# Kernel tuning notes

Hardware: AMD Instinct MI355X
Metric: run time of the kernel (lower is better)

The kernel has to match this reference:

```python
import math
import jax, jax.numpy as jnp
from jax import lax
import numpy as np

B, S, H, D = 2, 2048, 8, 32
Q_CHUNK = 64  # query-block size; keeps the [b,chunk,t,h,d] diff tensor ~256 MB


def setup_inputs() -> dict:
    key = jax.random.key(0)
    kq, kk = jax.random.split(key)
    q = jax.random.normal(kq, (B, S, H, D), dtype=jnp.float32)
    k = jax.random.normal(kk, (B, S, H, D), dtype=jnp.float32)
    return {"q": q, "k": k}


def _l1_scores(q, k):
    # q, k: [b, s, h, d] -> attn: [b, s, t, h]
    b, s, h, d = q.shape
    scale = 1.0 / math.sqrt(d)
    n_chunks = s // Q_CHUNK
    # [n_chunks, b, Q_CHUNK, h, d]
    q_blocks = jnp.moveaxis(q.reshape(b, n_chunks, Q_CHUNK, h, d), 1, 0)

    def step(carry, q_blk):
        # q_blk: [b, c, h, d]; k: [b, t, h, d]
        # diff: [b, c, t, h, d] -> reduce over d
        dist = jnp.sum(jnp.abs(q_blk[:, :, None, :, :] - k[:, None, :, :, :]), axis=-1)
        return carry, -dist * scale  # [b, c, t, h]

    _, out = lax.scan(step, None, q_blocks)  # [n_chunks, b, c, t, h]
    return jnp.moveaxis(out, 0, 1).reshape(b, s, s, h)


def reference(q, k):
    return _l1_scores(q, k)
```

## Files before the change

kernel.cpp:

```cpp
#include <hip/hip_runtime.h>
#include <cstdint>
#include <cstddef>


#define S_DIM 2048
#define H_DIM 8
#define D_DIM 32
#define RS 4
#define SB 16
#define TSPLIT 4
#define TCHUNK 8
#define NTHREADS 256
#define NCH ((S_DIM / TSPLIT) / TCHUNK)

typedef float f32x4 __attribute__((ext_vector_type(4)));

__global__ __launch_bounds__(NTHREADS) void l1attn_kernel(
    const float* __restrict__ q, const float* __restrict__ k,
    float* __restrict__ out)
{
  __shared__ float ldsk[TCHUNK * H_DIM * D_DIM];

  const int tid  = threadIdx.x;
  const int lane = tid & 63;
  const int wave = tid >> 6;

  const int bid = blockIdx.x;
  const int b   = bid >> 9;
  const int rem = bid & 511;
  const int sg  = rem >> 2;
  const int tq  = rem & 3;

  const int h      = lane & 7;
  const int t_sub  = lane >> 3;
  const int s_base = sg * SB + wave * RS;
  const int t0     = tq * (S_DIM / TSPLIT);

  f32x4 qf[RS][8];
  {
    const float* qb = q + (size_t)b * S_DIM * (H_DIM * D_DIM);
#pragma unroll
    for (int i = 0; i < RS; ++i) {
      const float* qr = qb + (size_t)(s_base + i) * (H_DIM * D_DIM) + h * D_DIM;
#pragma unroll
      for (int dv = 0; dv < 8; ++dv)
        qf[i][dv] = *(const f32x4*)(qr + dv * 4);
    }
  }

  const float* kb = k + (size_t)b * S_DIM * (H_DIM * D_DIM);

  const int g4a = tid;
  const int g4b = tid + 256;
  const int f4a = (g4a & 7) * 64 + (g4a >> 3);
  const int f4b = (g4b & 7) * 64 + (g4b >> 3);

  const f32x4* kc0 = (const f32x4*)(kb + (size_t)t0 * (H_DIM * D_DIM));
  f32x4 st0 = kc0[g4a];
  f32x4 st1 = kc0[g4b];

  const float nscale = -0.17677669529663687f;
  float* optr = out +
      ((size_t)(b * S_DIM + s_base) * S_DIM + (size_t)(t0 + t_sub)) * H_DIM + h;

  f32x4* ldsv = (f32x4*)ldsk;

  for (int c = 0; c < NCH; ++c) {
    __syncthreads();

    ldsv[f4a] = st0;
    ldsv[f4b] = st1;

    if (c + 1 < NCH) {
      const f32x4* kn = (const f32x4*)(kb +
          (size_t)(t0 + (c + 1) * TCHUNK) * (H_DIM * D_DIM));
      st0 = kn[g4a];
      st1 = kn[g4b];
    }

    __syncthreads();

    float acc0 = 0.f, acc1 = 0.f, acc2 = 0.f, acc3 = 0.f;
#pragma unroll
    for (int dv = 0; dv < 8; ++dv) {
      const f32x4 kf = ldsv[dv * 64 + lane];
      acc0 += __builtin_fabsf(qf[0][dv].x - kf.x) + __builtin_fabsf(qf[0][dv].y - kf.y)
            + __builtin_fabsf(qf[0][dv].z - kf.z) + __builtin_fabsf(qf[0][dv].w - kf.w);
      acc1 += __builtin_fabsf(qf[1][dv].x - kf.x) + __builtin_fabsf(qf[1][dv].y - kf.y)
            + __builtin_fabsf(qf[1][dv].z - kf.z) + __builtin_fabsf(qf[1][dv].w - kf.w);
      acc2 += __builtin_fabsf(qf[2][dv].x - kf.x) + __builtin_fabsf(qf[2][dv].y - kf.y)
            + __builtin_fabsf(qf[2][dv].z - kf.z) + __builtin_fabsf(qf[2][dv].w - kf.w);
      acc3 += __builtin_fabsf(qf[3][dv].x - kf.x) + __builtin_fabsf(qf[3][dv].y - kf.y)
            + __builtin_fabsf(qf[3][dv].z - kf.z) + __builtin_fabsf(qf[3][dv].w - kf.w);
    }

    float* o = optr + (size_t)c * (TCHUNK * H_DIM);
    o[0]                         = acc0 * nscale;
    o[(size_t)1 * S_DIM * H_DIM] = acc1 * nscale;
    o[(size_t)2 * S_DIM * H_DIM] = acc2 * nscale;
    o[(size_t)3 * S_DIM * H_DIM] = acc3 * nscale;
  }
}

extern "C" void kernel_launch(void* const* d_in, const int* in_sizes, int n_in,
                              void* d_out, int out_size, void* d_ws, size_t ws_size,
                              hipStream_t stream) {
  const float* q = (const float*)d_in[0];
  const float* k = (const float*)d_in[1];
  float* out = (float*)d_out;
  const int B = 2;
  dim3 grid(B * (S_DIM / SB) * TSPLIT);
  dim3 block(NTHREADS);
  l1attn_kernel<<<grid, block, 0, stream>>>(q, k, out);
}
```

Baseline: 375.2 us.

## Double-buffer K tiles in LDS, swizzle layout, and split keys eight ways

Replaces the single LDS K tile with two ping-pong buffers. Each iteration stages the next chunk while the current one is consumed, so one of the two barriers per iteration goes away. The LDS layout changes from a transposed store to a rotated (swizzled) row layout, which aims to cut bank conflicts on the staging writes. The key dimension is split eight ways instead of four, doubling the grid for more parallelism, at the cost of twice the LDS space per block and more Q reloads.

```diff
diff --git a/kernel.cpp b/kernel.cpp
--- a/kernel.cpp
+++ b/kernel.cpp
@@ -8,7 +8,7 @@
 #define D_DIM 32
 #define RS 4
 #define SB 16
-#define TSPLIT 4
+#define TSPLIT 8
 #define TCHUNK 8
 #define NTHREADS 256
 #define NCH ((S_DIM / TSPLIT) / TCHUNK)
@@ -19,17 +19,17 @@
     const float* __restrict__ q, const float* __restrict__ k,
     float* __restrict__ out)
 {
-  __shared__ float ldsk[TCHUNK * H_DIM * D_DIM];
+  __shared__ float ldsk[2][TCHUNK * H_DIM * D_DIM];
 
   const int tid  = threadIdx.x;
   const int lane = tid & 63;
   const int wave = tid >> 6;
 
   const int bid = blockIdx.x;
-  const int b   = bid >> 9;
-  const int rem = bid & 511;
-  const int sg  = rem >> 2;
-  const int tq  = rem & 3;
+  const int b   = bid >> 10;
+  const int rem = bid & 1023;
+  const int sg  = rem >> 3;
+  const int tq  = rem & 7;
 
   const int h      = lane & 7;
   const int t_sub  = lane >> 3;
@@ -52,38 +52,52 @@
 
   const int g4a = tid;
   const int g4b = tid + 256;
-  const int f4a = (g4a & 7) * 64 + (g4a >> 3);
-  const int f4b = (g4b & 7) * 64 + (g4b >> 3);
+  const int f4a = ((g4a >> 3) << 3) | (((g4a & 7) + (g4a >> 3)) & 7);
+  const int f4b = ((g4b >> 3) << 3) | (((g4b & 7) + (g4b >> 3)) & 7);
 
-  const f32x4* kc0 = (const f32x4*)(kb + (size_t)t0 * (H_DIM * D_DIM));
-  f32x4 st0 = kc0[g4a];
-  f32x4 st1 = kc0[g4b];
+  int raddr[8];
+#pragma unroll
+  for (int dv = 0; dv < 8; ++dv)
+    raddr[dv] = (lane << 3) | ((dv + lane) & 7);
+
+  f32x4 st0, st1;
+  {
+    const f32x4* kc0 = (const f32x4*)(kb + (size_t)t0 * (H_DIM * D_DIM));
+    st0 = kc0[g4a];
+    st1 = kc0[g4b];
+    f32x4* b0 = (f32x4*)ldsk[0];
+    b0[f4a] = st0;
+    b0[f4b] = st1;
+    const f32x4* kc1 = (const f32x4*)(kb +
+        (size_t)(t0 + TCHUNK) * (H_DIM * D_DIM));
+    st0 = kc1[g4a];
+    st1 = kc1[g4b];
+  }
 
   const float nscale = -0.17677669529663687f;
   float* optr = out +
       ((size_t)(b * S_DIM + s_base) * S_DIM + (size_t)(t0 + t_sub)) * H_DIM + h;
 
-  f32x4* ldsv = (f32x4*)ldsk;
-
   for (int c = 0; c < NCH; ++c) {
     __syncthreads();
 
-    ldsv[f4a] = st0;
-    ldsv[f4b] = st1;
-
     if (c + 1 < NCH) {
-      const f32x4* kn = (const f32x4*)(kb +
-          (size_t)(t0 + (c + 1) * TCHUNK) * (H_DIM * D_DIM));
-      st0 = kn[g4a];
-      st1 = kn[g4b];
+      f32x4* nb = (f32x4*)ldsk[(c + 1) & 1];
+      nb[f4a] = st0;
+      nb[f4b] = st1;
+      if (c + 2 < NCH) {
+        const f32x4* kn = (const f32x4*)(kb +
+            (size_t)(t0 + (c + 2) * TCHUNK) * (H_DIM * D_DIM));
+        st0 = kn[g4a];
+        st1 = kn[g4b];
+      }
     }
 
-    __syncthreads();
-
+    const f32x4* kp = (const f32x4*)ldsk[c & 1];
     float acc0 = 0.f, acc1 = 0.f, acc2 = 0.f, acc3 = 0.f;
 #pragma unroll
     for (int dv = 0; dv < 8; ++dv) {
-      const f32x4 kf = ldsv[dv * 64 + lane];
+      const f32x4 kf = kp[raddr[dv]];
       acc0 += __builtin_fabsf(qf[0][dv].x - kf.x) + __builtin_fabsf(qf[0][dv].y - kf.y)
             + __builtin_fabsf(qf[0][dv].z - kf.z) + __builtin_fabsf(qf[0][dv].w - kf.w);
       acc1 += __builtin_fabsf(qf[1][dv].x - kf.x) + __builtin_fabsf(qf[1][dv].y - kf.y)
```

After: 351.3 us. 6.4% less time.

## Use single-wave workgroups with private K staging and swizzled LDS layout

Applied to the files above, without the earlier changes.

Each 256-thread block with four waves sharing one K chunk becomes a single 64-lane wave. That wave loads the whole K chunk itself into a swizzled LDS layout meant to avoid bank conflicts. The two __syncthreads per chunk become wave barriers, and the grid is split eight ways along t instead of four. This removes cross-wave barrier stalls, but each wave now fetches its own K data, so K traffic to L2 rises about fourfold.

```diff
diff --git a/kernel.cpp b/kernel.cpp
--- a/kernel.cpp
+++ b/kernel.cpp
@@ -7,10 +7,9 @@
 #define H_DIM 8
 #define D_DIM 32
 #define RS 4
-#define SB 16
-#define TSPLIT 4
+#define TSPLIT 8
 #define TCHUNK 8
-#define NTHREADS 256
+#define NTHREADS 64
 #define NCH ((S_DIM / TSPLIT) / TCHUNK)
 
 typedef float f32x4 __attribute__((ext_vector_type(4)));
@@ -19,21 +18,18 @@
     const float* __restrict__ q, const float* __restrict__ k,
     float* __restrict__ out)
 {
-  __shared__ float ldsk[TCHUNK * H_DIM * D_DIM];
+  __shared__ f32x4 ldsk[TCHUNK * H_DIM * D_DIM / 4];
 
-  const int tid  = threadIdx.x;
-  const int lane = tid & 63;
-  const int wave = tid >> 6;
+  const int lane = threadIdx.x;
 
   const int bid = blockIdx.x;
-  const int b   = bid >> 9;
-  const int rem = bid & 511;
-  const int sg  = rem >> 2;
-  const int tq  = rem & 3;
+  const int b   = bid >> 12;
+  const int tq  = (bid >> 9) & 7;
+  const int sg  = bid & 511;
 
   const int h      = lane & 7;
   const int t_sub  = lane >> 3;
-  const int s_base = sg * SB + wave * RS;
+  const int s_base = sg * RS;
   const int t0     = tq * (S_DIM / TSPLIT);
 
   f32x4 qf[RS][8];
@@ -41,49 +37,53 @@
     const float* qb = q + (size_t)b * S_DIM * (H_DIM * D_DIM);
 #pragma unroll
     for (int i = 0; i < RS; ++i) {
-      const float* qr = qb + (size_t)(s_base + i) * (H_DIM * D_DIM) + h * D_DIM;
+      const f32x4* qr = (const f32x4*)(qb +
+          (size_t)(s_base + i) * (H_DIM * D_DIM) + h * D_DIM);
 #pragma unroll
       for (int dv = 0; dv < 8; ++dv)
-        qf[i][dv] = *(const f32x4*)(qr + dv * 4);
+        qf[i][dv] = qr[dv];
     }
   }
 
-  const float* kb = k + (size_t)b * S_DIM * (H_DIM * D_DIM);
+  const f32x4* kbv = (const f32x4*)(k + (size_t)b * S_DIM * (H_DIM * D_DIM));
 
-  const int g4a = tid;
-  const int g4b = tid + 256;
-  const int f4a = (g4a & 7) * 64 + (g4a >> 3);
-  const int f4b = (g4b & 7) * 64 + (g4b >> 3);
+  const int f4b0 = ((lane >> 3) << 3) | (((lane & 7) + (lane >> 3)) & 7);
 
-  const f32x4* kc0 = (const f32x4*)(kb + (size_t)t0 * (H_DIM * D_DIM));
-  f32x4 st0 = kc0[g4a];
-  f32x4 st1 = kc0[g4b];
+  int rd[8];
+#pragma unroll
+  for (int dv = 0; dv < 8; ++dv)
+    rd[dv] = (lane << 3) | ((dv + lane) & 7);
+
+  f32x4 st[8];
+  {
+    const f32x4* kc = kbv + ((size_t)t0 << 6);
+#pragma unroll
+    for (int j = 0; j < 8; ++j)
+      st[j] = kc[(j << 6) + lane];
+  }
 
   const float nscale = -0.17677669529663687f;
   float* optr = out +
       ((size_t)(b * S_DIM + s_base) * S_DIM + (size_t)(t0 + t_sub)) * H_DIM + h;
 
-  f32x4* ldsv = (f32x4*)ldsk;
+  for (int c = 0; c < NCH; ++c) {
+#pragma unroll
+    for (int j = 0; j < 8; ++j)
+      ldsk[(j << 6) + f4b0] = st[j];
 
-  for (int c = 0; c < NCH; ++c) {
-    __syncthreads();
-
-    ldsv[f4a] = st0;
-    ldsv[f4b] = st1;
+    __builtin_amdgcn_wave_barrier();
 
     if (c + 1 < NCH) {
-      const f32x4* kn = (const f32x4*)(kb +
-          (size_t)(t0 + (c + 1) * TCHUNK) * (H_DIM * D_DIM));
-      st0 = kn[g4a];
-      st1 = kn[g4b];
+      const f32x4* kn = kbv + ((size_t)(t0 + (c + 1) * TCHUNK) << 6);
+#pragma unroll
+      for (int j = 0; j < 8; ++j)
+        st[j] = kn[(j << 6) + lane];
     }
-
-    __syncthreads();
 
     float acc0 = 0.f, acc1 = 0.f, acc2 = 0.f, acc3 = 0.f;
 #pragma unroll
     for (int dv = 0; dv < 8; ++dv) {
-      const f32x4 kf = ldsv[dv * 64 + lane];
+      const f32x4 kf = ldsk[rd[dv]];
       acc0 += __builtin_fabsf(qf[0][dv].x - kf.x) + __builtin_fabsf(qf[0][dv].y - kf.y)
             + __builtin_fabsf(qf[0][dv].z - kf.z) + __builtin_fabsf(qf[0][dv].w - kf.w);
       acc1 += __builtin_fabsf(qf[1][dv].x - kf.x) + __builtin_fabsf(qf[1][dv].y - kf.y)
@@ -94,7 +94,9 @@
             + __builtin_fabsf(qf[3][dv].z - kf.z) + __builtin_fabsf(qf[3][dv].w - kf.w);
     }
 
-    float* o = optr + (size_t)c * (TCHUNK * H_DIM);
+    __builtin_amdgcn_wave_barrier();
+
+    float* o = optr + (size_t)(c << 6);
     o[0]                         = acc0 * nscale;
     o[(size_t)1 * S_DIM * H_DIM] = acc1 * nscale;
     o[(size_t)2 * S_DIM * H_DIM] = acc2 * nscale;
@@ -109,7 +111,8 @@
   const float* k = (const float*)d_in[1];
   float* out = (float*)d_out;
   const int B = 2;
-  dim3 grid(B * (S_DIM / SB) * TSPLIT);
+  dim3 grid(B * TSPLIT * (S_DIM / RS / NTHREADS * NTHREADS) / 64 * 64 / 8 * 8);
+  grid.x = B * TSPLIT * (S_DIM / RS);
   dim3 block(NTHREADS);
   l1attn_kernel<<<grid, block, 0, stream>>>(q, k, out);
 }
```

Result: slower. 423.7 us (+12.9%).
